# Kernel tuning notes

Hardware: AMD Instinct MI355X
Metric: run time of the kernel (lower is better)

## Reference

```python
import jax, jax.numpy as jnp
import numpy as np
from jax import lax

MAX_ID = 32        # instance ids in the 3d grid are 0..MAX_ID-1
NUM_CLASSES = 13   # semantic labels 0..12 (wall=10, floor=11)
RADIUS = 3
GRID = (256, 256, 256)
SURFACE_THRESH = 1.5
WALL_CLASS, WALL_ID = 10, 1
FLOOR_CLASS, FLOOR_ID = 11, 2
THINGS_START = 2

# offsets in the same lexicographic order as nn_search's triple loop: range(-R, R)
_r = np.arange(-RADIUS, RADIUS)
OFFSETS = np.stack(np.meshgrid(_r, _r, _r, indexing='ij'), -1).reshape(-1, 3).astype(np.int32)


def setup_inputs() -> dict:
    key = jax.random.key(0)
    k1, k2, k3, k4 = jax.random.split(key, 4)
    geometry = jax.random.normal(k1, GRID, dtype=jnp.float32)            # TSDF-like grid
    instances = jax.random.randint(k2, GRID, 0, MAX_ID, dtype=jnp.int32)
    semantics = jax.random.randint(k3, GRID, 0, NUM_CLASSES, dtype=jnp.int32)
    ids2d = jax.random.randint(k4, (16,), 0, MAX_ID, dtype=jnp.int32)    # instances2d['locations'][0]
    return {'geometry': geometry, 'instances': instances, 'semantics': semantics, 'ids2d': ids2d}


def _postprocess(geometry, instances, semantics, ids2d):
    inst_flat = instances.ravel()
    ids2d_p1 = ids2d + 1

    # filter_instances: keep only 3d ids present in (2d instance ids + 1)
    sel_mask = jnp.isin(instances, ids2d_p1)                 # filtered = instances * sel_mask
    zero_present = jnp.any(~sel_mask).astype(jnp.int32)      # does unique(filtered) contain 0?

    # per-id presence; panoptic id = (index of id in unique(filtered)) + THINGS_START
    hist = jnp.bincount(inst_flat, length=MAX_ID + 1)        # voxel count per id
    in2d = jnp.isin(jnp.arange(1, MAX_ID + 1), ids2d_p1)
    present = in2d & (hist[1:] > 0)                          # for ids 1..MAX_ID
    rank = jnp.cumsum(present.astype(jnp.int32))             # 1-based rank among present ids
    pano_ids = jnp.where(present, rank - 1 + zero_present + THINGS_START, 0)
    pano_lut = jnp.zeros(MAX_ID + 1, jnp.int32).at[1:].set(pano_ids)
    panoptic = pano_lut[instances]                           # assign per instances==id masks

    # majority semantic label per instance, excluding {0, wall, floor}
    counts = jnp.zeros((MAX_ID + 1, NUM_CLASSES), jnp.int32).at[inst_flat, semantics.ravel()].add(1)
    counts = counts.at[:, jnp.array([0, WALL_CLASS, FLOOR_CLASS])].set(-1)
    sel_label = jnp.argmax(counts[1:], axis=1).astype(jnp.int32)

    # stuff overrides
    panoptic = jnp.where(semantics == WALL_CLASS, WALL_ID, panoptic)
    panoptic = jnp.where(semantics == FLOOR_CLASS, FLOOR_ID, panoptic)

    surface = jnp.abs(geometry) <= SURFACE_THRESH
    unassigned = surface & (panoptic == 0)
    grid0 = panoptic                                          # panoptic_instances_copy

    def body(carry, off):
        label, found = carry
        shifted = jnp.roll(grid0, shift=-off, axis=(0, 1, 2))  # shifted[p] = grid0[p + off]
        new = (shifted > 0) & ~found
        return (jnp.where(new, shifted, label), found | new), None

    init = (jnp.zeros(GRID, jnp.int32), jnp.zeros(GRID, dtype=bool))
    (nn_label, _), _ = lax.scan(body, init, jnp.asarray(OFFSETS))
    panoptic = jnp.where(unassigned, nn_label, grid0)

    # panoptic id -> semantic label LUT (disjoint ids, order-independent)
    sem_lut = (jnp.zeros(MAX_ID + THINGS_START + 1, jnp.int32)
               .at[WALL_ID].set(WALL_CLASS).at[FLOOR_ID].set(FLOOR_CLASS))
    sem_lut = sem_lut.at[pano_ids].set(jnp.where(present, sel_label, 0))
    panoptic_semantics = sem_lut[panoptic]
    return panoptic, panoptic_semantics


def reference(geometry, instances, semantics, ids2d):
    return jax.jit(_postprocess)(geometry, instances, semantics, ids2d)
```

## Files before the change

kernel.cpp:

```cpp
#include <hip/hip_runtime.h>
#include <stdint.h>

#define GRID_N (256*256*256)
#define MAXID 32
#define NCLS 13
#define NBINS ((MAXID+1)*NCLS)


__global__ __launch_bounds__(256) void k_prep(const int* __restrict__ inst,
                                              const int* __restrict__ sem,
                                              int* __restrict__ counts,
                                              uint8_t* __restrict__ key) {
    __shared__ int sh[NBINS];
    for (int i = threadIdx.x; i < NBINS; i += blockDim.x) sh[i] = 0;
    __syncthreads();
    int tid = blockIdx.x * blockDim.x + threadIdx.x;
    int stride = gridDim.x * blockDim.x;
    const int n4 = GRID_N / 4;
    for (int i = tid; i < n4; i += stride) {
        int4 a = ((const int4*)inst)[i];
        int4 b = ((const int4*)sem)[i];
        atomicAdd(&sh[a.x * NCLS + b.x], 1);
        atomicAdd(&sh[a.y * NCLS + b.y], 1);
        atomicAdd(&sh[a.z * NCLS + b.z], 1);
        atomicAdd(&sh[a.w * NCLS + b.w], 1);
        uchar4 k;
        k.x = (b.x == 11) ? 33 : ((b.x == 10) ? 32 : (uint8_t)a.x);
        k.y = (b.y == 11) ? 33 : ((b.y == 10) ? 32 : (uint8_t)a.y);
        k.z = (b.z == 11) ? 33 : ((b.z == 10) ? 32 : (uint8_t)a.z);
        k.w = (b.w == 11) ? 33 : ((b.w == 10) ? 32 : (uint8_t)a.w);
        ((uchar4*)key)[i] = k;
    }
    __syncthreads();
    for (int i = threadIdx.x; i < NBINS; i += blockDim.x) {
        int v = sh[i];
        if (v) atomicAdd(&counts[i], v);
    }
}

__global__ __launch_bounds__(512) void k_luts(const int* __restrict__ counts,
                                              const int* __restrict__ ids2d, int n2d,
                                              int* __restrict__ glut) {
    __shared__ int shc[NBINS];
    __shared__ int hist[MAXID + 1];
    __shared__ int in2d[MAXID + 1];
    __shared__ int sel[MAXID + 1];
    int t = threadIdx.x;
    if (t < NBINS) shc[t] = counts[t];
    __syncthreads();
    if (t <= MAXID) {
        int s = 0;
        for (int c = 0; c < NCLS; ++c) s += shc[t * NCLS + c];
        hist[t] = s;
        int f = 0;
        for (int k = 0; k < n2d; ++k) if (ids2d[k] + 1 == t) f = 1;
        in2d[t] = f;
        int best = -2, bc = 0;
        for (int c = 0; c < NCLS; ++c) {
            int v = (c == 0 || c == 10 || c == 11) ? -1 : shc[t * NCLS + c];
            if (v > best) { best = v; bc = c; }
        }
        sel[t] = bc;
    }
    __syncthreads();
    if (t == 0) {
        int zero_present = 0;
        for (int i = 0; i <= MAXID; ++i)
            if (hist[i] > 0 && !in2d[i]) zero_present = 1;
        int pano_ids[MAXID + 1];
        int present[MAXID + 1];
        glut[0] = 0;
        int rank = 0;
        for (int j = 1; j <= MAXID; ++j) {
            int p = in2d[j] && (hist[j] > 0);
            present[j] = p;
            if (p) rank++;
            pano_ids[j] = p ? (rank - 1 + zero_present + 2) : 0;
            if (j < 32) glut[j] = pano_ids[j];
        }
        glut[32] = 1;
        glut[33] = 2;
        int* sem_lut = glut + 34;
        for (int i = 0; i < MAXID + 3; ++i) sem_lut[i] = 0;
        sem_lut[1] = 10;
        sem_lut[2] = 11;
        for (int j = 1; j <= MAXID; ++j)
            sem_lut[pano_ids[j]] = present[j] ? sel[j] : 0;
    }
}

#define ROWB 72
#define NROWS 81
#define NDW (NROWS*18)

__global__ __launch_bounds__(256) void k_nn(const float* __restrict__ geo,
                                            const uint8_t* __restrict__ key,
                                            const int* __restrict__ glut,
                                            int* __restrict__ out_pano,
                                            int* __restrict__ out_sem) {
    __shared__ uint8_t sh_g[NROWS * ROWB];
    __shared__ uint8_t sh_lut[64];
    __shared__ int slut[MAXID + 3];

    int t = threadIdx.x;
    if (t < 34) sh_lut[t] = (uint8_t)glut[t];
    else if (t >= 64 && t < 64 + MAXID + 3) slut[t - 64] = glut[34 + (t - 64)];
    __syncthreads();

    int z0 = blockIdx.x * 64;
    int y0 = blockIdx.y * 4;
    int x0 = blockIdx.z * 4;

    const uint32_t* key32 = (const uint32_t*)key;
    uint32_t* shg32 = (uint32_t*)sh_g;
    for (int idx = t; idx < NDW; idx += 256) {
        int row = idx / 18;
        int k = idx - row * 18;
        int ix = row / 9;
        int iy = row - ix * 9;
        int gx = (x0 + ix - 3) & 255;
        int gy = (y0 + iy - 3) & 255;
        int gzd = ((z0 - 4 + (k << 2)) & 255) >> 2;
        uint32_t w = key32[(gx << 14) | (gy << 6) | gzd];
        uint32_t g = (uint32_t)sh_lut[w & 63]
                   | ((uint32_t)sh_lut[(w >> 8) & 63] << 8)
                   | ((uint32_t)sh_lut[(w >> 16) & 63] << 16)
                   | ((uint32_t)sh_lut[(w >> 24) & 63] << 24);
        shg32[idx] = g;
    }
    __syncthreads();

    int tz = t & 63;
    int ty = t >> 6;
    const uint32_t* shr32 = (const uint32_t*)sh_g;

    for (int tx = 0; tx < 4; ++tx) {
        int x = x0 + tx, y = y0 + ty, z = z0 + tz;
        int i = (x << 16) | (y << 8) | z;
        int p = sh_g[((tx + 3) * 9 + (ty + 3)) * ROWB + tz + 4];
        float g = geo[i];
        if (p == 0 && fabsf(g) <= 1.5f) {
            int label = 0;
            for (int dxi = 0; dxi < 6 && !label; ++dxi) {
                int rb = ((tx + dxi) * 9 + ty) * ROWB + tz + 1;
                for (int dyi = 0; dyi < 6; ++dyi) {
                    int zb = rb + dyi * ROWB;
                    int a = zb >> 2, off = zb & 3;
                    uint32_t d0 = shr32[a], d1 = shr32[a + 1], d2 = shr32[a + 2];
                    uint64_t lo = (uint64_t)d0 | ((uint64_t)d1 << 32);
                    uint64_t win = lo >> (off * 8);
                    if (off) win |= (uint64_t)d2 << (64 - off * 8);
                    uint64_t mask = win & 0x0000FFFFFFFFFFFFULL;
                    if (mask) {
                        int b = __ffsll((long long)mask) - 1;
                        label = (int)((win >> (b & 56)) & 0xff);
                        break;
                    }
                }
            }
            p = label;
        }
        out_pano[i] = p;
        out_sem[i] = slut[p];
    }
}

extern "C" void kernel_launch(void* const* d_in, const int* in_sizes, int n_in,
                              void* d_out, int out_size, void* d_ws, size_t ws_size,
                              hipStream_t stream) {
    const float* geo   = (const float*)d_in[0];
    const int*   inst  = (const int*)d_in[1];
    const int*   sem   = (const int*)d_in[2];
    const int*   ids2d = (const int*)d_in[3];
    const int    n2d   = in_sizes[3];

    char* ws = (char*)d_ws;
    int* counts  = (int*)(ws);
    int* glut    = (int*)(ws + 4096);
    uint8_t* key = (uint8_t*)(ws + 16384);

    int* out_pano = (int*)d_out;
    int* out_sem  = out_pano + GRID_N;

    hipMemsetAsync(counts, 0, 4096, stream);
    k_prep<<<1024, 256, 0, stream>>>(inst, sem, counts, key);
    k_luts<<<1, 512, 0, stream>>>(counts, ids2d, n2d, glut);
    dim3 g(4, 64, 64);
    k_nn<<<g, 256, 0, stream>>>(geo, key, glut, out_pano, out_sem);
}
```

Before: 339.2 us.

## Pack surface bit into key, retile NN search to full-z 8x8 columns

The surface test |geo|<=1.5 moves into the prep pass and is stored as bit 6 of the byte key, so the NN kernel no longer reads geometry. The NN kernel now tiles full 256-long z columns over 8x8 xy blocks with 512 threads. That cuts halo overhead from 9x9x72 per 4x4x64 tile to 13x13x264 per 8x8x256, and each thread handles 4 voxels with int4 output stores. The prep histogram is split into two shared copies per block to reduce atomic contention. The trade-offs are larger shared memory per block and more serial search work per thread.

```diff
diff --git a/kernel.cpp b/kernel.cpp
--- a/kernel.cpp
+++ b/kernel.cpp
@@ -7,33 +7,36 @@
 #define NBINS ((MAXID+1)*NCLS)
 
 
-__global__ __launch_bounds__(256) void k_prep(const int* __restrict__ inst,
+__global__ __launch_bounds__(256) void k_prep(const float* __restrict__ geo,
+                                              const int* __restrict__ inst,
                                               const int* __restrict__ sem,
                                               int* __restrict__ counts,
                                               uint8_t* __restrict__ key) {
-    __shared__ int sh[NBINS];
-    for (int i = threadIdx.x; i < NBINS; i += blockDim.x) sh[i] = 0;
-    __syncthreads();
+    __shared__ int sh[2][NBINS];
+    for (int i = threadIdx.x; i < 2 * NBINS; i += blockDim.x) sh[0][i] = 0;
+    __syncthreads();
+    int* myh = sh[(threadIdx.x >> 6) & 1];
     int tid = blockIdx.x * blockDim.x + threadIdx.x;
     int stride = gridDim.x * blockDim.x;
     const int n4 = GRID_N / 4;
     for (int i = tid; i < n4; i += stride) {
         int4 a = ((const int4*)inst)[i];
         int4 b = ((const int4*)sem)[i];
-        atomicAdd(&sh[a.x * NCLS + b.x], 1);
-        atomicAdd(&sh[a.y * NCLS + b.y], 1);
-        atomicAdd(&sh[a.z * NCLS + b.z], 1);
-        atomicAdd(&sh[a.w * NCLS + b.w], 1);
+        float4 g = ((const float4*)geo)[i];
+        atomicAdd(&myh[a.x * NCLS + b.x], 1);
+        atomicAdd(&myh[a.y * NCLS + b.y], 1);
+        atomicAdd(&myh[a.z * NCLS + b.z], 1);
+        atomicAdd(&myh[a.w * NCLS + b.w], 1);
         uchar4 k;
-        k.x = (b.x == 11) ? 33 : ((b.x == 10) ? 32 : (uint8_t)a.x);
-        k.y = (b.y == 11) ? 33 : ((b.y == 10) ? 32 : (uint8_t)a.y);
-        k.z = (b.z == 11) ? 33 : ((b.z == 10) ? 32 : (uint8_t)a.z);
-        k.w = (b.w == 11) ? 33 : ((b.w == 10) ? 32 : (uint8_t)a.w);
+        k.x = ((b.x == 11) ? 33 : ((b.x == 10) ? 32 : (uint8_t)a.x)) | (fabsf(g.x) <= 1.5f ? 64 : 0);
+        k.y = ((b.y == 11) ? 33 : ((b.y == 10) ? 32 : (uint8_t)a.y)) | (fabsf(g.y) <= 1.5f ? 64 : 0);
+        k.z = ((b.z == 11) ? 33 : ((b.z == 10) ? 32 : (uint8_t)a.z)) | (fabsf(g.z) <= 1.5f ? 64 : 0);
+        k.w = ((b.w == 11) ? 33 : ((b.w == 10) ? 32 : (uint8_t)a.w)) | (fabsf(g.w) <= 1.5f ? 64 : 0);
         ((uchar4*)key)[i] = k;
     }
     __syncthreads();
     for (int i = threadIdx.x; i < NBINS; i += blockDim.x) {
-        int v = sh[i];
+        int v = sh[0][i] + sh[1][i];
         if (v) atomicAdd(&counts[i], v);
     }
 }
@@ -89,79 +92,94 @@
     }
 }
 
-#define ROWB 72
-#define NROWS 81
-#define NDW (NROWS*18)
-
-__global__ __launch_bounds__(256) void k_nn(const float* __restrict__ geo,
-                                            const uint8_t* __restrict__ key,
+#define TX 8
+#define TY 8
+#define HR 13
+#define NROWS (HR*HR)
+#define ROWDW 66
+#define NDW (NROWS*ROWDW)
+
+__global__ __launch_bounds__(512) void k_nn(const uint8_t* __restrict__ key,
                                             const int* __restrict__ glut,
                                             int* __restrict__ out_pano,
                                             int* __restrict__ out_sem) {
-    __shared__ uint8_t sh_g[NROWS * ROWB];
-    __shared__ uint8_t sh_lut[64];
+    __shared__ uint32_t shg[NDW];
+    __shared__ int lut[128];
     __shared__ int slut[MAXID + 3];
 
     int t = threadIdx.x;
-    if (t < 34) sh_lut[t] = (uint8_t)glut[t];
-    else if (t >= 64 && t < 64 + MAXID + 3) slut[t - 64] = glut[34 + (t - 64)];
-    __syncthreads();
-
-    int z0 = blockIdx.x * 64;
-    int y0 = blockIdx.y * 4;
-    int x0 = blockIdx.z * 4;
+    if (t < 128) {
+        int base = ((t & 63) <= 33) ? glut[t & 63] : 0;
+        lut[t] = base | ((t & 64) << 1);
+    } else if (t >= 128 && t < 128 + MAXID + 3) {
+        slut[t - 128] = glut[34 + (t - 128)];
+    }
+    __syncthreads();
+
+    int x0 = blockIdx.x * TX;
+    int y0 = blockIdx.y * TY;
 
     const uint32_t* key32 = (const uint32_t*)key;
-    uint32_t* shg32 = (uint32_t*)sh_g;
-    for (int idx = t; idx < NDW; idx += 256) {
-        int row = idx / 18;
-        int k = idx - row * 18;
-        int ix = row / 9;
-        int iy = row - ix * 9;
+    for (int idx = t; idx < NDW; idx += 512) {
+        int row = idx / ROWDW;
+        int k = idx - row * ROWDW;
+        int ix = row / HR;
+        int iy = row - ix * HR;
         int gx = (x0 + ix - 3) & 255;
         int gy = (y0 + iy - 3) & 255;
-        int gzd = ((z0 - 4 + (k << 2)) & 255) >> 2;
-        uint32_t w = key32[(gx << 14) | (gy << 6) | gzd];
-        uint32_t g = (uint32_t)sh_lut[w & 63]
-                   | ((uint32_t)sh_lut[(w >> 8) & 63] << 8)
-                   | ((uint32_t)sh_lut[(w >> 16) & 63] << 16)
-                   | ((uint32_t)sh_lut[(w >> 24) & 63] << 24);
-        shg32[idx] = g;
-    }
-    __syncthreads();
-
-    int tz = t & 63;
+        uint32_t w = key32[(gx << 14) | (gy << 6) | ((k - 1) & 63)];
+        shg[idx] = (uint32_t)lut[w & 127]
+                 | ((uint32_t)lut[(w >> 8) & 127] << 8)
+                 | ((uint32_t)lut[(w >> 16) & 127] << 16)
+                 | ((uint32_t)lut[(w >> 24) & 127] << 24);
+    }
+    __syncthreads();
+
+    int zg = t & 63;
     int ty = t >> 6;
-    const uint32_t* shr32 = (const uint32_t*)sh_g;
-
-    for (int tx = 0; tx < 4; ++tx) {
-        int x = x0 + tx, y = y0 + ty, z = z0 + tz;
-        int i = (x << 16) | (y << 8) | z;
-        int p = sh_g[((tx + 3) * 9 + (ty + 3)) * ROWB + tz + 4];
-        float g = geo[i];
-        if (p == 0 && fabsf(g) <= 1.5f) {
-            int label = 0;
-            for (int dxi = 0; dxi < 6 && !label; ++dxi) {
-                int rb = ((tx + dxi) * 9 + ty) * ROWB + tz + 1;
-                for (int dyi = 0; dyi < 6; ++dyi) {
-                    int zb = rb + dyi * ROWB;
-                    int a = zb >> 2, off = zb & 3;
-                    uint32_t d0 = shr32[a], d1 = shr32[a + 1], d2 = shr32[a + 2];
-                    uint64_t lo = (uint64_t)d0 | ((uint64_t)d1 << 32);
-                    uint64_t win = lo >> (off * 8);
-                    if (off) win |= (uint64_t)d2 << (64 - off * 8);
-                    uint64_t mask = win & 0x0000FFFFFFFFFFFFULL;
-                    if (mask) {
-                        int b = __ffsll((long long)mask) - 1;
-                        label = (int)((win >> (b & 56)) & 0xff);
-                        break;
+    int gy = y0 + ty;
+    const uint64_t M6 = 0x00007F7F7F7F7F7FULL;
+
+    for (int x = 0; x < TX; ++x) {
+        int gx = x0 + x;
+        int r0 = (x + 3) * HR + (ty + 3);
+        uint32_t cw = shg[r0 * ROWDW + zg + 1];
+        int4 pano, semv;
+        int pv[4];
+        #pragma unroll
+        for (int b = 0; b < 4; ++b) {
+            int v = (cw >> (8 * b)) & 255;
+            int p = v & 127;
+            if (p == 0 && (v & 128)) {
+                int z = 4 * zg + b;
+                int label = 0;
+                int j0 = z + 1;
+                int a0 = j0 >> 2, off = j0 & 3;
+                for (int dxi = 0; dxi < 6 && !label; ++dxi) {
+                    int rb = ((x + dxi) * HR + ty) * ROWDW + a0;
+                    for (int dyi = 0; dyi < 6; ++dyi) {
+                        int a = rb + dyi * ROWDW;
+                        uint32_t d0 = shg[a], d1 = shg[a + 1], d2 = shg[a + 2];
+                        uint64_t lo = (uint64_t)d0 | ((uint64_t)d1 << 32);
+                        uint64_t win = lo >> (off * 8);
+                        if (off) win |= (uint64_t)d2 << (64 - off * 8);
+                        uint64_t mask = win & M6;
+                        if (mask) {
+                            int bb = __ffsll((long long)mask) - 1;
+                            label = (int)((win >> (bb & 56)) & 0x7f);
+                            break;
+                        }
                     }
                 }
+                p = label;
             }
-            p = label;
+            pv[b] = p;
         }
-        out_pano[i] = p;
-        out_sem[i] = slut[p];
+        pano.x = pv[0]; pano.y = pv[1]; pano.z = pv[2]; pano.w = pv[3];
+        semv.x = slut[pv[0]]; semv.y = slut[pv[1]]; semv.z = slut[pv[2]]; semv.w = slut[pv[3]];
+        int oi = (gx << 14) | (gy << 6) | zg;
+        ((int4*)out_pano)[oi] = pano;
+        ((int4*)out_sem)[oi] = semv;
     }
 }
 
@@ -183,8 +201,8 @@
     int* out_sem  = out_pano + GRID_N;
 
     hipMemsetAsync(counts, 0, 4096, stream);
-    k_prep<<<1024, 256, 0, stream>>>(inst, sem, counts, key);
+    k_prep<<<1024, 256, 0, stream>>>(geo, inst, sem, counts, key);
     k_luts<<<1, 512, 0, stream>>>(counts, ids2d, n2d, glut);
-    dim3 g(4, 64, 64);
-    k_nn<<<g, 256, 0, stream>>>(geo, key, glut, out_pano, out_sem);
-}
+    dim3 g(32, 32);
+    k_nn<<<g, 512, 0, stream>>>(key, glut, out_pano, out_sem);
+}
```

Result: faster. 309.0 us (-8.9%).
